# Kernel optimization log

Measured on AMD Instinct MI355X. Metric: run time of the kernel, lower is better.

Reference implementation:

```python
import jax, jax.numpy as jnp
import numpy as np

B, D, C = 4096, 4096, 1024


def setup_inputs() -> dict:
    key = jax.random.key(0)
    kx, kw = jax.random.split(key)
    x = jax.random.normal(kx, (B, D), dtype=jnp.float32)
    # kaiming_normal_ with nonlinearity='relu': std = sqrt(2 / fan_in)
    W = jax.random.normal(kw, (C, D), dtype=jnp.float32) * jnp.sqrt(2.0 / D)
    return {"x": x, "W": W}


def reference(x, W):
    # Original: -( (x[:, :, None] - W.T[None, :, :])**2 ).mean(axis=1)
    d = x.shape[1]
    x_sq = jnp.sum(x * x, axis=1, keepdims=True)        # [B, 1]
    w_sq = jnp.sum(W * W, axis=1)[None, :]              # [1, C]
    cross = jnp.einsum('bd,cd->bc', x, W)               # [B, C] tensor-core GEMM
    return -(x_sq - 2.0 * cross + w_sq) / d
```

## Files before the change

kernel.cpp:

```cpp
#include <hip/hip_runtime.h>
#include <hip/hip_bf16.h>


typedef float f32x4 __attribute__((ext_vector_type(4)));
typedef float f32x2 __attribute__((ext_vector_type(2)));
typedef long long2_t __attribute__((ext_vector_type(2)));

#define BDIM 4096
#define DDIM 4096
#define CDIM 1024
#define TM 128
#define TN 128
#define BK 64
#define KSPLIT 4
#define NIT ((DDIM / KSPLIT) / BK)
#define SCALE 32.0f
#define INV_SS (1.0f/1024.0f)
#define PSCALE 0.0625f

#define SYNC_LGKM() asm volatile("s_waitcnt lgkmcnt(0)\n\ts_barrier" ::: "memory")

__global__ __launch_bounds__(256) void cvt_rowsq(
    const float* __restrict__ x, const float* __restrict__ W,
    unsigned char* __restrict__ xb, unsigned char* __restrict__ wb,
    float* __restrict__ xsq, float* __restrict__ wsq)
{
    const int lane = threadIdx.x & 63;
    const int row = blockIdx.x * 4 + (threadIdx.x >> 6);

    const float* src;
    unsigned char* dst;
    float* sq;
    if (row < BDIM) {
        src = x + (size_t)row * DDIM;
        dst = xb + (size_t)row * DDIM;
        sq = xsq + row;
    } else {
        int r = row - BDIM;
        src = W + (size_t)r * DDIM;
        dst = wb + (size_t)r * DDIM;
        sq = wsq + r;
    }

    const float4* s4 = (const float4*)src;
    unsigned int* d4 = (unsigned int*)dst;
    float a = 0.f;
    #pragma unroll
    for (int s = 0; s < DDIM / 4 / 64; ++s) {
        float4 f = s4[lane + 64 * s];
        a += f.x * f.x + f.y * f.y + f.z * f.z + f.w * f.w;
        unsigned int p = 0;
        p = __builtin_amdgcn_cvt_pk_fp8_f32(f.x * SCALE, f.y * SCALE, p, false);
        p = __builtin_amdgcn_cvt_pk_fp8_f32(f.z * SCALE, f.w * SCALE, p, true);
        d4[lane + 64 * s] = p;
    }
    #pragma unroll
    for (int off = 32; off > 0; off >>= 1) a += __shfl_down(a, off);
    if (lane == 0) *sq = a;
}

struct Pref { long2_t a0, a1, b0, b1; };

__global__ __launch_bounds__(256, 3) void gemm_eucl(
    const unsigned char* __restrict__ xb,
    const unsigned char* __restrict__ wb,
    unsigned int* __restrict__ part)
{
    __shared__ unsigned char sm[2 * 16384];

    const int tid = threadIdx.x;
    const int lane = tid & 63;
    const int wid = tid >> 6;
    const int bm = blockIdx.x * TM;
    const int bn = blockIdx.y * TN;
    const int ks = blockIdx.z * (DDIM / KSPLIT);
    const int wm = (wid >> 1) * 64;
    const int wn = (wid & 1) * 64;

    const int r0 = tid >> 2, c = tid & 3;
    const unsigned int oA0 = (unsigned int)((bm + r0) * DDIM + ks + c * 16);
    const unsigned int oA1 = oA0 + 64u * DDIM;
    const unsigned int oB0 = (unsigned int)((bn + r0) * DDIM + ks + c * 16);
    const unsigned int oB1 = oB0 + 64u * DDIM;

    const int k2o = (c >> 1) * 8;
    const int kcw = (c & 1) * 2;
    const int wo0 = r0 * 64 + ((kcw ^ (r0 & 3)) * 16) + k2o;
    const int wo1 = r0 * 64 + (((kcw | 1) ^ (r0 & 3)) * 16) + k2o;

    const int kc = lane >> 4;
    const int ml = lane & 15;
    int aoff[4], boff[4];
    #pragma unroll
    for (int i = 0; i < 4; ++i) {
        int m = wm + i * 16 + ml;
        aoff[i] = m * 64 + ((kc ^ (m & 3)) * 16);
        int n = wn + i * 16 + ml;
        boff[i] = n * 64 + ((kc ^ (n & 3)) * 16);
    }

    f32x4 acc[4][4] = {};

#define LOADSET(S, KT)                                                   \
    do {                                                                 \
        (S).a0 = *(const long2_t*)(xb + oA0 + (KT) * BK);                \
        (S).a1 = *(const long2_t*)(xb + oA1 + (KT) * BK);                \
        (S).b0 = *(const long2_t*)(wb + oB0 + (KT) * BK);                \
        (S).b1 = *(const long2_t*)(wb + oB1 + (KT) * BK);                \
    } while (0)

#define WRITESET(buf, S)                                                 \
    do {                                                                 \
        unsigned char* sA = sm + (buf) * 16384;                          \
        unsigned char* sB = sA + 8192;                                   \
        *(long*)(sA + wo0) = (S).a0.x; *(long*)(sA + wo1) = (S).a0.y;    \
        *(long*)(sA + wo0 + 4096) = (S).a1.x;                            \
        *(long*)(sA + wo1 + 4096) = (S).a1.y;                            \
        *(long*)(sB + wo0) = (S).b0.x; *(long*)(sB + wo1) = (S).b0.y;    \
        *(long*)(sB + wo0 + 4096) = (S).b1.x;                            \
        *(long*)(sB + wo1 + 4096) = (S).b1.y;                            \
    } while (0)

#define MFMA8(LA, I)                                                     \
    do {                                                                 \
        _Pragma("unroll")                                                \
        for (int j = 0; j < 4; ++j) {                                    \
            acc[I][j] = __builtin_amdgcn_mfma_f32_16x16x32_fp8_fp8(      \
                (LA).x, lb[j].x, acc[I][j], 0, 0, 0);                    \
            acc[I][j] = __builtin_amdgcn_mfma_f32_16x16x32_fp8_fp8(      \
                (LA).y, lb[j].y, acc[I][j], 0, 0, 0);                    \
        }                                                                \
    } while (0)

#define COMPUTE(buf)                                                     \
    do {                                                                 \
        const unsigned char* sA = sm + (buf) * 16384;                    \
        const unsigned char* sB = sA + 8192;                             \
        long2_t lb[4];                                                   \
        _Pragma("unroll")                                                \
        for (int j = 0; j < 4; ++j) lb[j] = *(const long2_t*)(sB + boff[j]); \
        long2_t laA = *(const long2_t*)(sA + aoff[0]);                   \
        long2_t laB = *(const long2_t*)(sA + aoff[1]);                   \
        MFMA8(laA, 0);                                                   \
        laA = *(const long2_t*)(sA + aoff[2]);                           \
        MFMA8(laB, 1);                                                   \
        laB = *(const long2_t*)(sA + aoff[3]);                           \
        MFMA8(laA, 2);                                                   \
        MFMA8(laB, 3);                                                   \
    } while (0)

    Pref S[3];
    LOADSET(S[0], 0);
    LOADSET(S[1], 1);
    LOADSET(S[2], 2);
    WRITESET(0, S[0]);
    SYNC_LGKM();

    #pragma unroll
    for (int k = 0; k < NIT - 1; ++k) {
        if (k < NIT - 3) LOADSET(S[k % 3], k + 3);
        COMPUTE(k & 1);
        WRITESET((k + 1) & 1, S[(k + 1) % 3]);
        SYNC_LGKM();
    }
    COMPUTE((NIT - 1) & 1);

    unsigned int* p = part
        + (((size_t)blockIdx.z * 256 + (blockIdx.x * 8 + blockIdx.y)) * 16) * 256;
    #pragma unroll
    for (int i = 0; i < 4; ++i)
        #pragma unroll
        for (int j = 0; j < 4; ++j) {
            unsigned int pk = 0;
            pk = __builtin_amdgcn_cvt_pk_fp8_f32(
                acc[i][j][0] * PSCALE, acc[i][j][1] * PSCALE, pk, false);
            pk = __builtin_amdgcn_cvt_pk_fp8_f32(
                acc[i][j][2] * PSCALE, acc[i][j][3] * PSCALE, pk, true);
            p[(i * 4 + j) * 256 + tid] = pk;
        }
#undef LOADSET
#undef WRITESET
#undef MFMA8
#undef COMPUTE
}

__global__ __launch_bounds__(256) void reduce_out(
    const unsigned int* __restrict__ part, const float* __restrict__ xsq,
    const float* __restrict__ wsq, float* __restrict__ out)
{
    const int bid = blockIdx.x;
    const int bb = bid >> 1;
    const int f0 = (bid & 1) * 8;
    const int t = threadIdx.x;
    const int lane = t & 63;
    const int wid = t >> 6;
    const int bm = (bb >> 3) * TM, bn = (bb & 7) * TN;
    const int wm = (wid >> 1) * 64, wn = (wid & 1) * 64;
    const int row_l = (lane >> 4) * 4, col_l = lane & 15;
    const size_t sl = (size_t)256 * 16 * 256;
    const float c1 = 2.0f * 16.0f * INV_SS / (float)DDIM;
    const float c2 = 1.0f / (float)DDIM;

    #pragma unroll
    for (int f = f0; f < f0 + 8; ++f) {
        size_t o = ((size_t)bb * 16 + f) * 256 + t;
        f32x2 s01 = {0.f, 0.f}, s23 = {0.f, 0.f};
        #pragma unroll
        for (int z = 0; z < KSPLIT; ++z) {
            unsigned int u = part[o + (size_t)z * sl];
            s01 += __builtin_amdgcn_cvt_pk_f32_fp8(u, false);
            s23 += __builtin_amdgcn_cvt_pk_f32_fp8(u, true);
        }
        int i = f >> 2, j = f & 3;
        int gn = bn + wn + j * 16 + col_l;
        float wv = wsq[gn];
        float sv[4] = {s01.x, s01.y, s23.x, s23.y};
        #pragma unroll
        for (int r = 0; r < 4; ++r) {
            int gm = bm + wm + i * 16 + row_l + r;
            out[(size_t)gm * CDIM + gn] = sv[r] * c1 - (xsq[gm] + wv) * c2;
        }
    }
}

__global__ void fallback_kernel(const float* __restrict__ x, const float* __restrict__ W,
                                float* __restrict__ out)
{
    int c = blockIdx.x * blockDim.x + threadIdx.x;
    int b = blockIdx.y;
    if (c >= CDIM) return;
    const float* xr = x + (size_t)b * DDIM;
    const float* wr = W + (size_t)c * DDIM;
    float xs = 0.f, ws = 0.f, cr = 0.f;
    for (int d = 0; d < DDIM; ++d) {
        float xv = xr[d], wv = wr[d];
        xs += xv * xv; ws += wv * wv; cr += xv * wv;
    }
    out[(size_t)b * CDIM + c] = (2.0f * cr - xs - ws) / (float)DDIM;
}

extern "C" void kernel_launch(void* const* d_in, const int* in_sizes, int n_in,
                              void* d_out, int out_size, void* d_ws, size_t ws_size,
                              hipStream_t stream) {
    const float* x = (const float*)d_in[0];
    const float* W = (const float*)d_in[1];
    float* out = (float*)d_out;

    size_t need = (size_t)(BDIM + CDIM) * DDIM
                + (size_t)(BDIM + CDIM) * sizeof(float)
                + (size_t)KSPLIT * BDIM * CDIM;
    if (ws_size < need) {
        fallback_kernel<<<dim3(CDIM / 256, BDIM), 256, 0, stream>>>(x, W, out);
        return;
    }

    unsigned char* xb = (unsigned char*)d_ws;
    unsigned char* wb = xb + (size_t)BDIM * DDIM;
    float* xsq = (float*)(wb + (size_t)CDIM * DDIM);
    float* wsq = xsq + BDIM;
    unsigned int* part = (unsigned int*)(wsq + CDIM);

    cvt_rowsq<<<(BDIM + CDIM) / 4, 256, 0, stream>>>(x, W, xb, wb, xsq, wsq);
    gemm_eucl<<<dim3(BDIM / TM, CDIM / TN, KSPLIT), 256, 0, stream>>>(xb, wb, part);
    reduce_out<<<512, 256, 0, stream>>>(part, xsq, wsq, out);
}
```

Before: 142.3 us.

## Give each wave private LDS tiles to drop block barriers and halve K-split

Each wave now loads its own 64-row slices of A and B from global memory into a private double-buffered LDS region, so the block-wide s_barrier per K step is removed. KSPLIT drops from 4 to 2, which halves the fp8 partial-sum traffic and the reduce work; the partial scale changes to match. The three-deep register prefetch becomes one-deep and the occupancy hint drops from 3 to 2. In exchange each tile row is fetched by two waves, doubling global/L2 load traffic, and the grid is halved to 512 blocks with longer K loops.

Measured after the change: 159.4 us. +12.0%, slower.

```diff
diff --git a/kernel.cpp b/kernel.cpp
--- a/kernel.cpp
+++ b/kernel.cpp
@@ -12,13 +12,12 @@
 #define TM 128
 #define TN 128
 #define BK 64
-#define KSPLIT 4
+#define KSPLIT 2
 #define NIT ((DDIM / KSPLIT) / BK)
 #define SCALE 32.0f
 #define INV_SS (1.0f/1024.0f)
-#define PSCALE 0.0625f
-
-#define SYNC_LGKM() asm volatile("s_waitcnt lgkmcnt(0)\n\ts_barrier" ::: "memory")
+#define PSCALE (1.0f/32.0f)
+#define PS_INV 32.0f
 
 __global__ __launch_bounds__(256) void cvt_rowsq(
     const float* __restrict__ x, const float* __restrict__ W,
@@ -59,14 +58,14 @@
     if (lane == 0) *sq = a;
 }
 
-struct Pref { long2_t a0, a1, b0, b1; };
-
-__global__ __launch_bounds__(256, 3) void gemm_eucl(
+struct Pref { long2_t a[4], b[4]; };
+
+__global__ __launch_bounds__(256, 2) void gemm_eucl(
     const unsigned char* __restrict__ xb,
     const unsigned char* __restrict__ wb,
     unsigned int* __restrict__ part)
 {
-    __shared__ unsigned char sm[2 * 16384];
+    __shared__ unsigned char sm[4][2][8192];
 
     const int tid = threadIdx.x;
     const int lane = tid & 63;
@@ -77,91 +76,84 @@
     const int wm = (wid >> 1) * 64;
     const int wn = (wid & 1) * 64;
 
-    const int r0 = tid >> 2, c = tid & 3;
-    const unsigned int oA0 = (unsigned int)((bm + r0) * DDIM + ks + c * 16);
-    const unsigned int oA1 = oA0 + 64u * DDIM;
-    const unsigned int oB0 = (unsigned int)((bn + r0) * DDIM + ks + c * 16);
-    const unsigned int oB1 = oB0 + 64u * DDIM;
-
-    const int k2o = (c >> 1) * 8;
-    const int kcw = (c & 1) * 2;
-    const int wo0 = r0 * 64 + ((kcw ^ (r0 & 3)) * 16) + k2o;
-    const int wo1 = r0 * 64 + (((kcw | 1) ^ (r0 & 3)) * 16) + k2o;
+    const int lr = lane >> 2, c = lane & 3;
+    const unsigned char* gA[4];
+    const unsigned char* gB[4];
+    #pragma unroll
+    for (int q = 0; q < 4; ++q) {
+        gA[q] = xb + (size_t)(bm + wm + lr + 16 * q) * DDIM + ks + c * 16;
+        gB[q] = wb + (size_t)(bn + wn + lr + 16 * q) * DDIM + ks + c * 16;
+    }
+
+    unsigned char* mybuf = &sm[wid][0][0];
+    const int wbase = lr * 64 + ((c ^ (lr & 3)) * 16);
 
     const int kc = lane >> 4;
     const int ml = lane & 15;
     int aoff[4], boff[4];
     #pragma unroll
     for (int i = 0; i < 4; ++i) {
-        int m = wm + i * 16 + ml;
-        aoff[i] = m * 64 + ((kc ^ (m & 3)) * 16);
-        int n = wn + i * 16 + ml;
-        boff[i] = n * 64 + ((kc ^ (n & 3)) * 16);
+        int r = i * 16 + ml;
+        aoff[i] = r * 64 + ((kc ^ (r & 3)) * 16);
+        boff[i] = 4096 + aoff[i];
     }
 
     f32x4 acc[4][4] = {};
 
-#define LOADSET(S, KT)                                                   \
-    do {                                                                 \
-        (S).a0 = *(const long2_t*)(xb + oA0 + (KT) * BK);                \
-        (S).a1 = *(const long2_t*)(xb + oA1 + (KT) * BK);                \
-        (S).b0 = *(const long2_t*)(wb + oB0 + (KT) * BK);                \
-        (S).b1 = *(const long2_t*)(wb + oB1 + (KT) * BK);                \
-    } while (0)
-
-#define WRITESET(buf, S)                                                 \
-    do {                                                                 \
-        unsigned char* sA = sm + (buf) * 16384;                          \
-        unsigned char* sB = sA + 8192;                                   \
-        *(long*)(sA + wo0) = (S).a0.x; *(long*)(sA + wo1) = (S).a0.y;    \
-        *(long*)(sA + wo0 + 4096) = (S).a1.x;                            \
-        *(long*)(sA + wo1 + 4096) = (S).a1.y;                            \
-        *(long*)(sB + wo0) = (S).b0.x; *(long*)(sB + wo1) = (S).b0.y;    \
-        *(long*)(sB + wo0 + 4096) = (S).b1.x;                            \
-        *(long*)(sB + wo1 + 4096) = (S).b1.y;                            \
-    } while (0)
-
-#define MFMA8(LA, I)                                                     \
-    do {                                                                 \
-        _Pragma("unroll")                                                \
-        for (int j = 0; j < 4; ++j) {                                    \
-            acc[I][j] = __builtin_amdgcn_mfma_f32_16x16x32_fp8_fp8(      \
-                (LA).x, lb[j].x, acc[I][j], 0, 0, 0);                    \
-            acc[I][j] = __builtin_amdgcn_mfma_f32_16x16x32_fp8_fp8(      \
-                (LA).y, lb[j].y, acc[I][j], 0, 0, 0);                    \
-        }                                                                \
-    } while (0)
-
-#define COMPUTE(buf)                                                     \
-    do {                                                                 \
-        const unsigned char* sA = sm + (buf) * 16384;                    \
-        const unsigned char* sB = sA + 8192;                             \
-        long2_t lb[4];                                                   \
-        _Pragma("unroll")                                                \
-        for (int j = 0; j < 4; ++j) lb[j] = *(const long2_t*)(sB + boff[j]); \
-        long2_t laA = *(const long2_t*)(sA + aoff[0]);                   \
-        long2_t laB = *(const long2_t*)(sA + aoff[1]);                   \
-        MFMA8(laA, 0);                                                   \
-        laA = *(const long2_t*)(sA + aoff[2]);                           \
-        MFMA8(laB, 1);                                                   \
-        laB = *(const long2_t*)(sA + aoff[3]);                           \
-        MFMA8(laA, 2);                                                   \
-        MFMA8(laB, 3);                                                   \
-    } while (0)
-
-    Pref S[3];
-    LOADSET(S[0], 0);
-    LOADSET(S[1], 1);
-    LOADSET(S[2], 2);
-    WRITESET(0, S[0]);
-    SYNC_LGKM();
-
-    #pragma unroll
+#define LOADSET(S, KT)                                                    \
+    do {                                                                  \
+        _Pragma("unroll")                                                 \
+        for (int q = 0; q < 4; ++q) {                                     \
+            (S).a[q] = *(const long2_t*)(gA[q] + (KT) * BK);              \
+            (S).b[q] = *(const long2_t*)(gB[q] + (KT) * BK);              \
+        }                                                                 \
+    } while (0)
+
+#define WRITESET(buf, S)                                                  \
+    do {                                                                  \
+        unsigned char* d = mybuf + (buf) * 8192 + wbase;                  \
+        _Pragma("unroll")                                                 \
+        for (int q = 0; q < 4; ++q) {                                     \
+            *(long2_t*)(d + q * 1024) = (S).a[q];                         \
+            *(long2_t*)(d + q * 1024 + 4096) = (S).b[q];                  \
+        }                                                                 \
+    } while (0)
+
+#define MFMA8(LA, I)                                                      \
+    do {                                                                  \
+        _Pragma("unroll")                                                 \
+        for (int j = 0; j < 4; ++j) {                                     \
+            acc[I][j] = __builtin_amdgcn_mfma_f32_16x16x32_fp8_fp8(       \
+                (LA).x, lb[j].x, acc[I][j], 0, 0, 0);                     \
+            acc[I][j] = __builtin_amdgcn_mfma_f32_16x16x32_fp8_fp8(       \
+                (LA).y, lb[j].y, acc[I][j], 0, 0, 0);                     \
+        }                                                                 \
+    } while (0)
+
+#define COMPUTE(buf)                                                      \
+    do {                                                                  \
+        const unsigned char* s = mybuf + (buf) * 8192;                    \
+        long2_t lb[4];                                                    \
+        _Pragma("unroll")                                                 \
+        for (int j = 0; j < 4; ++j) lb[j] = *(const long2_t*)(s + boff[j]); \
+        long2_t laA = *(const long2_t*)(s + aoff[0]);                     \
+        long2_t laB = *(const long2_t*)(s + aoff[1]);                     \
+        MFMA8(laA, 0);                                                    \
+        laA = *(const long2_t*)(s + aoff[2]);                             \
+        MFMA8(laB, 1);                                                    \
+        laB = *(const long2_t*)(s + aoff[3]);                             \
+        MFMA8(laA, 2);                                                    \
+        MFMA8(laB, 3);                                                    \
+    } while (0)
+
+    Pref S;
+    LOADSET(S, 0);
+    WRITESET(0, S);
+    #pragma unroll 2
     for (int k = 0; k < NIT - 1; ++k) {
-        if (k < NIT - 3) LOADSET(S[k % 3], k + 3);
+        LOADSET(S, k + 1);
         COMPUTE(k & 1);
-        WRITESET((k + 1) & 1, S[(k + 1) % 3]);
-        SYNC_LGKM();
+        WRITESET((k + 1) & 1, S);
     }
     COMPUTE((NIT - 1) & 1);
 
@@ -198,7 +190,7 @@
     const int wm = (wid >> 1) * 64, wn = (wid & 1) * 64;
     const int row_l = (lane >> 4) * 4, col_l = lane & 15;
     const size_t sl = (size_t)256 * 16 * 256;
-    const float c1 = 2.0f * 16.0f * INV_SS / (float)DDIM;
+    const float c1 = 2.0f * PS_INV * INV_SS / (float)DDIM;
     const float c2 = 1.0f / (float)DDIM;
 
     #pragma unroll
```
